# Kernel tuning notes

Hardware: AMD Instinct MI355X
Metric: run time of the kernel (lower is better)

The kernel has to match this reference:

```python
import jax, jax.numpy as jnp
import numpy as np

B, D, NUM_IDS = 4096, 256, 100000
MARGIN = 0.5


def setup_inputs() -> dict:
    key = jax.random.key(0)
    k1, k2, k3, k4 = jax.random.split(key, 4)
    ftr = jax.random.normal(k1, (B, D), dtype=jnp.float32)
    teachor_ftr = jax.random.normal(k2, (B, D), dtype=jnp.float32)
    prototypes = jax.random.normal(k3, (NUM_IDS, D), dtype=jnp.float32)
    label = jax.random.randint(k4, (B,), 0, NUM_IDS, dtype=jnp.int64)
    return {"ftr": ftr, "teachor_ftr": teachor_ftr, "prototypes": prototypes, "label": label}


def reference(ftr, teachor_ftr, prototypes, label):
    # y = prototypes[label] : [B, D]
    y = prototypes[label]
    # similarity = ftr @ ftr.T : [B, B]
    sim = jnp.einsum('bd,kd->bk', ftr, ftr)
    n = ftr.shape[0]
    idx = jnp.arange(n)
    # Original: ascending sort, take first batch index i with i != label[row].
    # Equivalent: argmin of sim with positions where batch-index == label masked out.
    masked = jnp.where(idx[None, :] == label[:, None], jnp.inf, sim)
    neg_i = jnp.argmin(masked, axis=1)          # [B]
    neg = ftr[neg_i]                            # [B, D]
    pos_d = jnp.sum((ftr - y) ** 2, axis=1)     # [B]
    neg_d = jnp.sum((ftr - neg) ** 2, axis=1)   # [B]
    losses = jax.nn.relu(pos_d - neg_d + MARGIN)
    # sum(losses) / len(losses)
    return jnp.mean(losses)
```

## Files before the change

kernel.cpp:

```cpp
#include <hip/hip_runtime.h>
#include <hip/hip_bf16.h>
#include <stdint.h>


typedef __bf16 bf16_t;
typedef __bf16 bf16x8 __attribute__((ext_vector_type(8)));
typedef float f32x4 __attribute__((ext_vector_type(4)));

__device__ __forceinline__ unsigned int float_key(float x) {
    unsigned int u = __float_as_uint(x);
    return (u & 0x80000000u) ? ~u : (u | 0x80000000u);
}

__device__ __forceinline__ unsigned long long shfl_xor_u64(unsigned long long v, int mask) {
    unsigned int lo = (unsigned int)(v & 0xFFFFFFFFULL);
    unsigned int hi = (unsigned int)(v >> 32);
    lo = __shfl_xor(lo, mask, 64);
    hi = __shfl_xor(hi, mask, 64);
    return ((unsigned long long)hi << 32) | (unsigned long long)lo;
}

__device__ __forceinline__ void async_load16(const void* g, void* lds) {
    __builtin_amdgcn_global_load_lds(
        (__attribute__((address_space(1))) void*)(g),
        (__attribute__((address_space(3))) void*)(lds),
        16, 0, 0);
}

__global__ void init_kernel(unsigned long long* __restrict__ best, float* __restrict__ out, int B) {
    int i = blockIdx.x * blockDim.x + threadIdx.x;
    if (i < B) best[i] = 0xFFFFFFFFFFFFFFFFULL;
    if (i == 0) out[0] = 0.0f;
}

__global__ __launch_bounds__(256) void prep_kernel(
    const float* __restrict__ x, bf16_t* __restrict__ A2, bf16_t* __restrict__ B2,
    int B, int D)
{
    int i = blockIdx.x * blockDim.x + threadIdx.x;
    if (i >= B * D) return;
    int r = i / D, c = i - r * D;
    float v = x[i];
    bf16_t hi = (bf16_t)v;
    bf16_t lo = (bf16_t)(v - (float)hi);
    size_t base = (size_t)r * (3 * D);
    A2[base + c] = hi; A2[base + D + c] = hi; A2[base + 2 * D + c] = lo;
    B2[base + c] = hi; B2[base + D + c] = lo; B2[base + 2 * D + c] = hi;
}

__global__ __launch_bounds__(256, 3) void sim_mfma_kernel(
    const bf16_t* __restrict__ A2, const bf16_t* __restrict__ B2,
    const int* __restrict__ label, unsigned long long* __restrict__ best,
    int B, int K)
{
    __shared__ __align__(16) bf16_t sA[128 * 64];
    __shared__ __align__(16) bf16_t sB[128 * 64];
    __shared__ int sLab[128];

    const int tid  = threadIdx.x;
    const int lane = tid & 63;
    const int w    = tid >> 6;
    const int row0 = blockIdx.y * 128;
    const int col0 = blockIdx.x * 128;

    if (tid < 128) sLab[tid] = label[row0 + tid];

    const int srow   = w * 32 + (lane >> 3);
    const int schunk = ((lane & 7) ^ (lane >> 3)) << 3;
    const bf16_t* gA = A2 + (size_t)(row0 + srow) * K + schunk;
    const bf16_t* gB = B2 + (size_t)(col0 + srow) * K + schunk;
    bf16_t* lA0 = sA + (w * 32) * 64;
    bf16_t* lB0 = sB + (w * 32) * 64;

    f32x4 acc[4][4];
#pragma unroll
    for (int i = 0; i < 4; ++i)
#pragma unroll
        for (int j = 0; j < 4; ++j) acc[i][j] = (f32x4){0.f, 0.f, 0.f, 0.f};

    const int wr = (w >> 1) * 64;
    const int wc = (w & 1) * 64;
    const int qk = lane >> 4;
    const int ln = lane & 15;

    for (int k0 = 0; k0 < K; k0 += 64) {
        __syncthreads();
#pragma unroll
        for (int t = 0; t < 4; ++t) {
            async_load16(gA + (size_t)(t * 8) * K + k0, lA0 + t * 8 * 64);
            async_load16(gB + (size_t)(t * 8) * K + k0, lB0 + t * 8 * 64);
        }
        __syncthreads();

#pragma unroll
        for (int kk = 0; kk < 2; ++kk) {
            const int q  = kk * 4 + qk;
            const int cs = ((q ^ (ln & 7)) << 3);
            bf16x8 aF[4], bF[4];
#pragma unroll
            for (int f = 0; f < 4; ++f) {
                const int lrA = wr + f * 16 + ln;
                const int lrB = wc + f * 16 + ln;
                aF[f] = __builtin_bit_cast(bf16x8, *(const uint4*)&sA[lrA * 64 + cs]);
                bF[f] = __builtin_bit_cast(bf16x8, *(const uint4*)&sB[lrB * 64 + cs]);
            }
#pragma unroll
            for (int i = 0; i < 4; ++i)
#pragma unroll
                for (int j = 0; j < 4; ++j)
                    acc[i][j] = __builtin_amdgcn_mfma_f32_16x16x32_bf16(
                        aF[i], bF[j], acc[i][j], 0, 0, 0);
        }
    }

#pragma unroll
    for (int i = 0; i < 4; ++i) {
#pragma unroll
        for (int reg = 0; reg < 4; ++reg) {
            const int lr  = wr + i * 16 + qk * 4 + reg;
            const int r   = row0 + lr;
            const int lab = sLab[lr];
            unsigned long long bl = 0xFFFFFFFFFFFFFFFFULL;
#pragma unroll
            for (int j = 0; j < 4; ++j) {
                const int c = col0 + wc + j * 16 + ln;
                unsigned long long key =
                    ((unsigned long long)float_key(acc[i][j][reg]) << 32) | (unsigned int)c;
                if (c != lab && key < bl) bl = key;
            }
#pragma unroll
            for (int off = 1; off < 16; off <<= 1) {
                unsigned long long o = shfl_xor_u64(bl, off);
                if (o < bl) bl = o;
            }
            if (ln == 0) atomicMin(&best[r], bl);
        }
    }
}

__global__ __launch_bounds__(256) void loss_kernel(
    const float* __restrict__ ftr, const float* __restrict__ proto,
    const int* __restrict__ label, const unsigned long long* __restrict__ best,
    float* __restrict__ out, int B, int D, float inv_b)
{
    const int gid  = blockIdx.x * blockDim.x + threadIdx.x;
    const int row  = gid >> 6;
    const int lane = gid & 63;
    if (row >= B) return;

    const int lab = label[row];
    const int neg = (int)(unsigned int)(best[row] & 0xFFFFFFFFULL);

    float pd = 0.0f, nd = 0.0f;
    for (int d = lane * 4; d < D; d += 256) {
        float4 f = *(const float4*)(ftr   + (size_t)row * D + d);
        float4 y = *(const float4*)(proto + (size_t)lab * D + d);
        float4 n = *(const float4*)(ftr   + (size_t)neg * D + d);
        float dx = f.x - y.x, dy = f.y - y.y, dz = f.z - y.z, dw = f.w - y.w;
        pd += dx * dx + dy * dy + dz * dz + dw * dw;
        dx = f.x - n.x; dy = f.y - n.y; dz = f.z - n.z; dw = f.w - n.w;
        nd += dx * dx + dy * dy + dz * dz + dw * dw;
    }
#pragma unroll
    for (int off = 32; off >= 1; off >>= 1) {
        pd += __shfl_xor(pd, off, 64);
        nd += __shfl_xor(nd, off, 64);
    }
    if (lane == 0) {
        float l = pd - nd + 0.5f;
        if (l > 0.0f) atomicAdd(out, l * inv_b);
    }
}

extern "C" void kernel_launch(void* const* d_in, const int* in_sizes, int n_in,
                              void* d_out, int out_size, void* d_ws, size_t ws_size,
                              hipStream_t stream) {
    const float* ftr   = (const float*)d_in[0];
    const float* proto = (const float*)d_in[2];
    const int*   label = (const int*)d_in[3];

    const int B = in_sizes[3];
    const int D = in_sizes[0] / B;
    const int K = 3 * D;

    unsigned long long* best = (unsigned long long*)d_ws;
    size_t off = ((size_t)B * 8 + 255) & ~(size_t)255;
    bf16_t* A2 = (bf16_t*)((char*)d_ws + off);
    bf16_t* B2 = A2 + (size_t)B * K;

    float* out = (float*)d_out;

    init_kernel<<<(B + 255) / 256, 256, 0, stream>>>(best, out, B);
    prep_kernel<<<(B * D + 255) / 256, 256, 0, stream>>>(ftr, A2, B2, B, D);

    dim3 grid(B / 128, B / 128);
    sim_mfma_kernel<<<grid, 256, 0, stream>>>(A2, B2, label, best, B, K);

    loss_kernel<<<(B * 64 + 255) / 256, 256, 0, stream>>>(ftr, proto, label, best, out, B, D,
                                                          1.0f / (float)B);
}
```

Baseline: 179.5 us.

## Use single-pass fp16 MFMA and compute only upper-triangular similarity tiles

Replaces the three-term bf16 hi/lo split (K=3D) with a single fp16 copy of the features (K=D). It also launches only the upper-triangular 128x128 tiles of the symmetric Gram matrix, and each tile updates both its row and its column argmin through atomicMin. Init work is folded into the prep kernel, which now does vectorized float4-to-half conversion. Together these cut the MFMA work and the prep traffic. The cost is precision: fp16 dot products are less accurate than the split scheme, which could change argmin picks on near-ties. Each tile also does an extra column-reduction epilogue.

```diff
diff --git a/kernel.cpp b/kernel.cpp
--- a/kernel.cpp
+++ b/kernel.cpp
@@ -3,21 +3,24 @@
 #include <stdint.h>
 
 
-typedef __bf16 bf16_t;
-typedef __bf16 bf16x8 __attribute__((ext_vector_type(8)));
+typedef _Float16 f16;
+typedef _Float16 f16x4 __attribute__((ext_vector_type(4)));
+typedef _Float16 f16x8 __attribute__((ext_vector_type(8)));
 typedef float f32x4 __attribute__((ext_vector_type(4)));
-
-__device__ __forceinline__ unsigned int float_key(float x) {
+typedef unsigned long long u64;
+
+__device__ __forceinline__ u64 float_key(float x) {
     unsigned int u = __float_as_uint(x);
-    return (u & 0x80000000u) ? ~u : (u | 0x80000000u);
-}
-
-__device__ __forceinline__ unsigned long long shfl_xor_u64(unsigned long long v, int mask) {
+    u = (u & 0x80000000u) ? ~u : (u | 0x80000000u);
+    return (u64)u;
+}
+
+__device__ __forceinline__ u64 shfl_xor_u64(u64 v, int mask) {
     unsigned int lo = (unsigned int)(v & 0xFFFFFFFFULL);
     unsigned int hi = (unsigned int)(v >> 32);
     lo = __shfl_xor(lo, mask, 64);
     hi = __shfl_xor(hi, mask, 64);
-    return ((unsigned long long)hi << 32) | (unsigned long long)lo;
+    return ((u64)hi << 32) | (u64)lo;
 }
 
 __device__ __forceinline__ void async_load16(const void* g, void* lds) {
@@ -27,50 +30,52 @@
         16, 0, 0);
 }
 
-__global__ void init_kernel(unsigned long long* __restrict__ best, float* __restrict__ out, int B) {
-    int i = blockIdx.x * blockDim.x + threadIdx.x;
-    if (i < B) best[i] = 0xFFFFFFFFFFFFFFFFULL;
-    if (i == 0) out[0] = 0.0f;
-}
-
 __global__ __launch_bounds__(256) void prep_kernel(
-    const float* __restrict__ x, bf16_t* __restrict__ A2, bf16_t* __restrict__ B2,
-    int B, int D)
+    const float* __restrict__ x, f16* __restrict__ F,
+    u64* __restrict__ best, float* __restrict__ out, int B, int D)
 {
-    int i = blockIdx.x * blockDim.x + threadIdx.x;
-    if (i >= B * D) return;
-    int r = i / D, c = i - r * D;
-    float v = x[i];
-    bf16_t hi = (bf16_t)v;
-    bf16_t lo = (bf16_t)(v - (float)hi);
-    size_t base = (size_t)r * (3 * D);
-    A2[base + c] = hi; A2[base + D + c] = hi; A2[base + 2 * D + c] = lo;
-    B2[base + c] = hi; B2[base + D + c] = lo; B2[base + 2 * D + c] = hi;
+    int gid = blockIdx.x * blockDim.x + threadIdx.x;
+    int n4 = (B * D) >> 2;
+    if (gid < n4) {
+        float4 v = ((const float4*)x)[gid];
+        f16x4 h = { (f16)v.x, (f16)v.y, (f16)v.z, (f16)v.w };
+        ((f16x4*)F)[gid] = h;
+    }
+    if (gid < B) best[gid] = ~0ULL;
+    if (gid == 0) out[0] = 0.0f;
 }
 
 __global__ __launch_bounds__(256, 3) void sim_mfma_kernel(
-    const bf16_t* __restrict__ A2, const bf16_t* __restrict__ B2,
-    const int* __restrict__ label, unsigned long long* __restrict__ best,
-    int B, int K)
+    const f16* __restrict__ F, const int* __restrict__ label,
+    u64* __restrict__ best, int B, int K)
 {
-    __shared__ __align__(16) bf16_t sA[128 * 64];
-    __shared__ __align__(16) bf16_t sB[128 * 64];
-    __shared__ int sLab[128];
+    __shared__ __align__(16) f16 sA[128 * 64];
+    __shared__ __align__(16) f16 sB[128 * 64];
+    __shared__ int sLabR[128];
+    __shared__ int sLabC[128];
+
+    int bi = blockIdx.x;
+    int by = (int)((sqrtf(8.0f * (float)bi + 1.0f) - 1.0f) * 0.5f);
+    while ((by + 1) * (by + 2) / 2 <= bi) ++by;
+    while (by * (by + 1) / 2 > bi) --by;
+    const int bx = bi - by * (by + 1) / 2;
+
+    const int row0 = by * 128;
+    const int col0 = bx * 128;
 
     const int tid  = threadIdx.x;
     const int lane = tid & 63;
     const int w    = tid >> 6;
-    const int row0 = blockIdx.y * 128;
-    const int col0 = blockIdx.x * 128;
-
-    if (tid < 128) sLab[tid] = label[row0 + tid];
+
+    if (tid < 128) sLabR[tid] = label[row0 + tid];
+    else           sLabC[tid - 128] = label[col0 + (tid - 128)];
 
     const int srow   = w * 32 + (lane >> 3);
     const int schunk = ((lane & 7) ^ (lane >> 3)) << 3;
-    const bf16_t* gA = A2 + (size_t)(row0 + srow) * K + schunk;
-    const bf16_t* gB = B2 + (size_t)(col0 + srow) * K + schunk;
-    bf16_t* lA0 = sA + (w * 32) * 64;
-    bf16_t* lB0 = sB + (w * 32) * 64;
+    const f16* gA = F + (size_t)(row0 + srow) * K + schunk;
+    const f16* gB = F + (size_t)(col0 + srow) * K + schunk;
+    f16* lA0 = sA + (w * 32) * 64;
+    f16* lB0 = sB + (w * 32) * 64;
 
     f32x4 acc[4][4];
 #pragma unroll
@@ -96,19 +101,19 @@
         for (int kk = 0; kk < 2; ++kk) {
             const int q  = kk * 4 + qk;
             const int cs = ((q ^ (ln & 7)) << 3);
-            bf16x8 aF[4], bF[4];
+            f16x8 aF[4], bF[4];
 #pragma unroll
             for (int f = 0; f < 4; ++f) {
                 const int lrA = wr + f * 16 + ln;
                 const int lrB = wc + f * 16 + ln;
-                aF[f] = __builtin_bit_cast(bf16x8, *(const uint4*)&sA[lrA * 64 + cs]);
-                bF[f] = __builtin_bit_cast(bf16x8, *(const uint4*)&sB[lrB * 64 + cs]);
+                aF[f] = __builtin_bit_cast(f16x8, *(const uint4*)&sA[lrA * 64 + cs]);
+                bF[f] = __builtin_bit_cast(f16x8, *(const uint4*)&sB[lrB * 64 + cs]);
             }
 #pragma unroll
             for (int i = 0; i < 4; ++i)
 #pragma unroll
                 for (int j = 0; j < 4; ++j)
-                    acc[i][j] = __builtin_amdgcn_mfma_f32_16x16x32_bf16(
+                    acc[i][j] = __builtin_amdgcn_mfma_f32_16x16x32_f16(
                         aF[i], bF[j], acc[i][j], 0, 0, 0);
         }
     }
@@ -118,29 +123,49 @@
 #pragma unroll
         for (int reg = 0; reg < 4; ++reg) {
             const int lr  = wr + i * 16 + qk * 4 + reg;
-            const int r   = row0 + lr;
-            const int lab = sLab[lr];
-            unsigned long long bl = 0xFFFFFFFFFFFFFFFFULL;
+            const int lab = sLabR[lr];
+            u64 bl = ~0ULL;
 #pragma unroll
             for (int j = 0; j < 4; ++j) {
                 const int c = col0 + wc + j * 16 + ln;
-                unsigned long long key =
-                    ((unsigned long long)float_key(acc[i][j][reg]) << 32) | (unsigned int)c;
+                u64 key = (float_key(acc[i][j][reg]) << 32) | (unsigned int)c;
                 if (c != lab && key < bl) bl = key;
             }
 #pragma unroll
             for (int off = 1; off < 16; off <<= 1) {
-                unsigned long long o = shfl_xor_u64(bl, off);
+                u64 o = shfl_xor_u64(bl, off);
                 if (o < bl) bl = o;
             }
-            if (ln == 0) atomicMin(&best[r], bl);
-        }
+            if (ln == 0) atomicMin(&best[row0 + lr], bl);
+        }
+    }
+
+#pragma unroll
+    for (int j = 0; j < 4; ++j) {
+        const int cl  = wc + j * 16 + ln;
+        const int lab = sLabC[cl];
+        u64 bl = ~0ULL;
+#pragma unroll
+        for (int i = 0; i < 4; ++i) {
+#pragma unroll
+            for (int reg = 0; reg < 4; ++reg) {
+                const int rg = row0 + wr + i * 16 + qk * 4 + reg;
+                u64 key = (float_key(acc[i][j][reg]) << 32) | (unsigned int)rg;
+                if (rg != lab && key < bl) bl = key;
+            }
+        }
+#pragma unroll
+        for (int off = 16; off < 64; off <<= 1) {
+            u64 o = shfl_xor_u64(bl, off);
+            if (o < bl) bl = o;
+        }
+        if (qk == 0) atomicMin(&best[col0 + cl], bl);
     }
 }
 
 __global__ __launch_bounds__(256) void loss_kernel(
     const float* __restrict__ ftr, const float* __restrict__ proto,
-    const int* __restrict__ label, const unsigned long long* __restrict__ best,
+    const int* __restrict__ label, const u64* __restrict__ best,
     float* __restrict__ out, int B, int D, float inv_b)
 {
     const int gid  = blockIdx.x * blockDim.x + threadIdx.x;
@@ -181,20 +206,18 @@
 
     const int B = in_sizes[3];
     const int D = in_sizes[0] / B;
-    const int K = 3 * D;
-
-    unsigned long long* best = (unsigned long long*)d_ws;
+
+    u64* best = (u64*)d_ws;
     size_t off = ((size_t)B * 8 + 255) & ~(size_t)255;
-    bf16_t* A2 = (bf16_t*)((char*)d_ws + off);
-    bf16_t* B2 = A2 + (size_t)B * K;
-
+    f16* F = (f16*)((char*)d_ws + off);
     float* out = (float*)d_out;
 
-    init_kernel<<<(B + 255) / 256, 256, 0, stream>>>(best, out, B);
-    prep_kernel<<<(B * D + 255) / 256, 256, 0, stream>>>(ftr, A2, B2, B, D);
-
-    dim3 grid(B / 128, B / 128);
-    sim_mfma_kernel<<<grid, 256, 0, stream>>>(A2, B2, label, best, B, K);
+    const int prep_threads = (B * D) >> 2;
+    prep_kernel<<<(prep_threads + 255) / 256, 256, 0, stream>>>(ftr, F, best, out, B, D);
+
+    const int nb = B / 128;
+    const int ntri = nb * (nb + 1) / 2;
+    sim_mfma_kernel<<<ntri, 256, 0, stream>>>(F, label, best, B, D);
 
     loss_kernel<<<(B * 64 + 255) / 256, 256, 0, stream>>>(ftr, proto, label, best, out, B, D,
                                                           1.0f / (float)B);
```

After: 152.9 us. 14.8% less time.
